# Kernel optimization log

Measured on AMD Instinct MI355X. Metric: run time of the kernel, lower is better.

The kernel has to match this reference:

```python
import jax, jax.numpy as jnp
import numpy as np

S = 100        # sos_token_num
H = 12         # num heads
LY = 3         # number of residual blocks
NEG = -100.0   # attention-bias masking value


def layer_norm(x, w, b, eps=1e-5):
    u = jnp.mean(x, -1, keepdims=True)
    v = jnp.mean((x - u) ** 2, -1, keepdims=True)
    return (x - u) / jnp.sqrt(v + eps) * w + b


def quick_gelu(x):
    return x * jax.nn.sigmoid(1.702 * x)


def l2norm(x, eps=1e-12):
    return x / jnp.maximum(jnp.linalg.norm(x, axis=-1, keepdims=True), eps)


def setup_inputs() -> dict:
    key = jax.random.key(0)
    ks = iter(jax.random.split(key, 32))
    n, c, hh, ww, out_dim = 2, 768, 32, 32, 512
    r = lambda shape, s=1.0: jax.random.normal(next(ks), shape, jnp.float32) * s
    return dict(
        cls_token=r((1, n, c)),
        pix_feat=r((n, c, hh, ww)),
        last_surgery=r((1 + hh * ww, n, c)),
        attn_bias=r((n, 1, S, hh, ww)),
        qkv_w=r((LY, 3 * c, c), 0.02), qkv_b=jnp.zeros((LY, 3 * c)),
        proj_w=r((LY, c, c), 0.02), proj_b=jnp.zeros((LY, c)),
        ln1_w=jnp.ones((LY, c)), ln1_b=jnp.zeros((LY, c)),
        ln2_w=jnp.ones((LY, c)), ln2_b=jnp.zeros((LY, c)),
        fc_w=r((LY, 4 * c, c), 0.02), fc_b=jnp.zeros((LY, 4 * c)),
        fc2_w=r((LY, c, 4 * c), 0.02), fc2_b=jnp.zeros((LY, c)),
        lnp_w=jnp.ones((c,)), lnp_b=jnp.zeros((c,)),
        proj_out=r((c, out_dim), 0.02),
    )


def reference(cls_token, pix_feat, last_surgery, attn_bias,
              qkv_w, qkv_b, proj_w, proj_b,
              ln1_w, ln1_b, ln2_w, ln2_b,
              fc_w, fc_b, fc2_w, fc2_b,
              lnp_w, lnp_b, proj_out):
    n, c, hh, ww = pix_feat.shape
    L = hh * ww
    N = S + 1 + L
    d = c // H
    scale = d ** -0.5

    # ---- assemble token streams (batch-first [n, N, c]) ----
    pix_tok = pix_feat.reshape(n, c, L).transpose(2, 0, 1)          # [L, n, c]
    x = jnp.concatenate([jnp.broadcast_to(cls_token, (S, n, c)), cls_token, pix_tok], 0)
    x_sur = jnp.concatenate([jnp.broadcast_to(last_surgery[0:1], (S, n, c)), last_surgery], 0)
    xo = x.transpose(1, 0, 2)      # 'original' stream  [n, N, c]
    xs = x_sur.transpose(1, 0, 2)  # 'surgery'  stream  [n, N, c]

    # ---- build attention biases (identity downsample: bias already at (h, w)) ----
    base = jnp.zeros((N, N), jnp.float32)
    base = base.at[:, :S].set(NEG)
    base = base.at[jnp.arange(S), jnp.arange(S)].set(0.0)
    base = base.at[:S, S].set(NEG)
    plain = jnp.broadcast_to(base, (n, H, N, N))
    bias = jnp.broadcast_to(attn_bias, (n, H, S, hh, ww)).reshape(n, H, S, L)
    biased = plain.at[:, :, :S, S + 1:].set(bias)   # sos rows attend to pixels via bias

    def attention(t, l):
        # t: [n, N, c] (post-ln_1); returns (surgery_res, ori_res)
        qkv = (t @ qkv_w[l].T + qkv_b[l]).reshape(n, N, 3, H, d).transpose(2, 0, 3, 1, 4)
        q, k, v = qkv[0], qkv[1], qkv[2]   # each [n, H, N, d]
        def attend(q_, k_, mask):
            a = jax.nn.softmax(jnp.einsum('bhnd,bhmd->bhnm', q_, k_) * scale + mask, axis=-1)
            o = jnp.einsum('bhnm,bhmd->bhnd', a, v).transpose(0, 2, 1, 3).reshape(n, N, c)
            return o @ proj_w[l].T + proj_b[l]
        x_ori_res = attend(q, k, biased)   # standard pass, biased mask (attn_mask[0])
        x_res = attend(v, v, plain)        # q = k = v surgery pass (attn_mask[1])
        return x_res, x_ori_res

    for l in range(LY):
        t = layer_norm(xo, ln1_w[l], ln1_b[l])
        res_sur, res_ori = attention(t, l)
        xo = xo + res_ori
        xo = xo + (quick_gelu(layer_norm(xo, ln2_w[l], ln2_b[l]) @ fc_w[l].T + fc_b[l]) @ fc2_w[l].T + fc2_b[l])
        xs = xs + res_sur

    # ---- heads ----
    sos = l2norm(layer_norm(xo[:, :S], lnp_w, lnp_b) @ proj_out)          # [n, S, out]
    img = l2norm(layer_norm(xs[:, S:], lnp_w, lnp_b) @ proj_out)          # [n, 1+L, out]
    img = img[:, 1:, :].transpose(0, 2, 1).reshape(n, proj_out.shape[1], hh, ww)
    return sos, img
```

## Files before the change

kernel.cpp:

```cpp
#include <hip/hip_runtime.h>
#include <math.h>


constexpr int Cc = 768;
constexpr int Ss = 100;
constexpr int Hh = 12;
constexpr int Ll = 1024;
constexpr int Nn = 1125;
constexpr int NB = 2;
constexpr int VTS = 1216;
constexpr float QS = 0.18033688011112042f;
constexpr float LOG2E = 1.4426950408889634f;

typedef unsigned short u16;
typedef unsigned int u32;
typedef __attribute__((ext_vector_type(8))) short short8v;
typedef __attribute__((ext_vector_type(8))) unsigned short ushort8v;
typedef __attribute__((ext_vector_type(4))) float f32x4;
typedef __attribute__((ext_vector_type(4))) unsigned int u32x4;

__device__ inline u16 f2bf(float f) {
  unsigned u = __builtin_bit_cast(unsigned int, f);
  unsigned r = u + 0x7fffu + ((u >> 16) & 1u);
  return (u16)(r >> 16);
}
__device__ inline float bf2f(u16 v) {
  return __builtin_bit_cast(float, (unsigned int)v << 16);
}
__device__ inline unsigned cvtpk(float lo, float hi) {
  unsigned r;
  asm("v_cvt_pk_bf16_f32 %0, %1, %2" : "=v"(r) : "v"(lo), "v"(hi));
  return r;
}
__device__ inline float max3f(float a, float b, float c) {
  float r;
  asm("v_max3_f32 %0, %1, %2, %3" : "=v"(r) : "v"(a), "v"(b), "v"(c));
  return r;
}
__device__ __forceinline__ void gl_lds16(const u16* g, u16* l) {
  __builtin_amdgcn_global_load_lds(
      (const __attribute__((address_space(1))) u32*)g,
      (__attribute__((address_space(3))) u32*)l, 16, 0, 0);
}

__device__ inline int swz(int row, int col) {
  return (row << 6) + ((((col >> 3) ^ (row & 7)) << 3) | (col & 7));
}

__global__ __launch_bounds__(256) void assemble_kernel(
    const float* __restrict__ cls, const float* __restrict__ pix,
    const float* __restrict__ sur, float* __restrict__ xo, float* __restrict__ xs) {
  int idx = blockIdx.x * 256 + (int)threadIdx.x;
  int total = NB * Nn * Cc;
  if (idx >= total) return;
  int ch = idx % Cc;
  int t  = (idx / Cc) % Nn;
  int b  = idx / (Cc * Nn);
  float vo, vs;
  if (t <= Ss) vo = cls[b * Cc + ch];
  else         vo = pix[(size_t)b * Cc * Ll + (size_t)ch * Ll + (t - Ss - 1)];
  if (t < Ss)  vs = sur[b * Cc + ch];
  else         vs = sur[(size_t)(t - Ss) * NB * Cc + b * Cc + ch];
  xo[idx] = vo;
  xs[idx] = vs;
}

constexpr int CN0 = 3 * 2304 * 768;
constexpr int CN1 = 3 * 768 * 768;
constexpr int CN2 = 3 * 3072 * 768;
constexpr int CN3 = 3 * 768 * 3072;
__global__ __launch_bounds__(256) void cvt4_kernel(
    const float* __restrict__ s0, const float* __restrict__ s1,
    const float* __restrict__ s2, const float* __restrict__ s3,
    u16* __restrict__ dst) {
  int i4 = (blockIdx.x * 256 + (int)threadIdx.x) * 4;
  if (i4 >= CN0 + CN1 + CN2 + CN3) return;
  const float* src; int off;
  if (i4 < CN0)             { src = s0; off = i4; }
  else if (i4 < CN0 + CN1)  { src = s1; off = i4 - CN0; }
  else if (i4 < CN0 + CN1 + CN2) { src = s2; off = i4 - CN0 - CN1; }
  else                      { src = s3; off = i4 - CN0 - CN1 - CN2; }
  float4 v = *(const float4*)(src + off);
  *(ushort4*)(dst + i4) = make_ushort4(f2bf(v.x), f2bf(v.y), f2bf(v.z), f2bf(v.w));
}

__global__ __launch_bounds__(256) void transpose_po_kernel(
    const float* __restrict__ in, u16* __restrict__ out) {
  int id = blockIdx.x * 256 + (int)threadIdx.x;
  if (id >= 512 * 768) return;
  int nidx = id / 768, k = id - nidx * 768;
  out[id] = f2bf(in[(size_t)k * 512 + nidx]);
}

__global__ __launch_bounds__(256) void vtrans_kernel(
    const u16* __restrict__ qkv, u16* __restrict__ vtg) {
  __shared__ u16 tile[64][72];
  int tt = blockIdx.x;
  int bh = blockIdx.y;
  int b = bh / Hh, h = bh - b * Hh;
  int tid = (int)threadIdx.x;
  {
    int tl = tid >> 2, c0 = (tid & 3) << 4;
    int tok = tt * 64 + tl;
    int tokc = tok > 1124 ? 1124 : tok;
    const u16* src = qkv + ((size_t)(b * Nn + tokc)) * 2304 + 2 * Cc + h * 64 + c0;
    ushort8v v0 = *(const ushort8v*)src;
    ushort8v v1 = *(const ushort8v*)(src + 8);
    if (tok > 1124) { v0 = (ushort8v)0; v1 = (ushort8v)0; }
    *(ushort8v*)&tile[tl][c0] = v0;
    *(ushort8v*)&tile[tl][c0 + 8] = v1;
  }
  __syncthreads();
  {
    int d = tid >> 2, t0 = (tid & 3) << 4;
    ushort8v o0, o1;
#pragma unroll
    for (int j = 0; j < 8; ++j) { o0[j] = tile[t0 + j][d]; o1[j] = tile[t0 + 8 + j][d]; }
    size_t orow = ((size_t)bh * 64 + d) * VTS + tt * 64 + t0;
    *(ushort8v*)&vtg[orow] = o0;
    *(ushort8v*)&vtg[orow + 8] = o1;
  }
}

__global__ __launch_bounds__(256) void ln_kernel(
    const float* __restrict__ X, const float* __restrict__ w, const float* __restrict__ b,
    u16* __restrict__ Y, int rows_per_b, int row_off) {
  int r = blockIdx.x;
  int bb = r / rows_per_b;
  int i  = r % rows_per_b;
  const float* x = X + ((size_t)bb * Nn + row_off + i) * Cc;
  u16* y = Y + (size_t)r * Cc;
  int tid = (int)threadIdx.x;
  float v0 = x[tid], v1 = x[tid + 256], v2 = x[tid + 512];
  float s = v0 + v1 + v2;
  __shared__ float sbuf[4];
  for (int off = 32; off; off >>= 1) s += __shfl_xor(s, off);
  if ((tid & 63) == 0) sbuf[tid >> 6] = s;
  __syncthreads();
  float mean = (sbuf[0] + sbuf[1] + sbuf[2] + sbuf[3]) * (1.0f / Cc);
  float d0 = v0 - mean, d1 = v1 - mean, d2 = v2 - mean;
  float q = d0 * d0 + d1 * d1 + d2 * d2;
  __syncthreads();
  for (int off = 32; off; off >>= 1) q += __shfl_xor(q, off);
  if ((tid & 63) == 0) sbuf[tid >> 6] = q;
  __syncthreads();
  float var = (sbuf[0] + sbuf[1] + sbuf[2] + sbuf[3]) * (1.0f / Cc);
  float inv = rsqrtf(var + 1e-5f);
  y[tid]       = f2bf(d0 * inv * w[tid]       + b[tid]);
  y[tid + 256] = f2bf(d1 * inv * w[tid + 256] + b[tid + 256]);
  y[tid + 512] = f2bf(d2 * inv * w[tid + 512] + b[tid + 512]);
}

__global__ __launch_bounds__(256) void gemm64_kernel(
    const u16* __restrict__ A0, const u16* __restrict__ A1,
    const u16* __restrict__ B, const float* __restrict__ bias,
    const float* __restrict__ res0, const float* __restrict__ res1,
    float* __restrict__ outf0, float* __restrict__ outf1,
    u16* __restrict__ outb0, u16* __restrict__ outb1,
    int M, int N, int K, int act) {
  __shared__ __align__(16) u16 Als[64 * 64];
  __shared__ __align__(16) u16 Bls[128 * 64];
  int zz = blockIdx.z;
  const u16* A = zz ? A1 : A0;
  const float* res = zz ? res1 : res0;
  float* outf = zz ? outf1 : outf0;
  u16* outb = zz ? outb1 : outb0;
  int tid = (int)threadIdx.x;
  int wave = tid >> 6, lane = tid & 63, g = lane >> 4, li = lane & 15;
  int row0 = blockIdx.y * 64, col0 = blockIdx.x * 128;

  int lr = lane >> 3, lc = (lane & 7) << 3;
  int ar0 = row0 + wave * 16 + lr;      if (ar0 > M - 1) ar0 = M - 1;
  int ar1 = row0 + wave * 16 + 8 + lr;  if (ar1 > M - 1) ar1 = M - 1;
  const u16* as0 = A + (size_t)ar0 * K + lc;
  const u16* as1 = A + (size_t)ar1 * K + lc;
  u16* al0 = &Als[wave * 1024];
  u16* al1 = &Als[wave * 1024 + 512];
  const u16* bs[4]; u16* bl[4];
#pragma unroll
  for (int j = 0; j < 4; ++j) {
    int brow = wave * 32 + j * 8 + lr;
    bs[j] = B + (size_t)(col0 + brow) * K + lc;
    bl[j] = &Bls[(wave * 4 + j) * 512];
  }

  f32x4 acc[4][2];
#pragma unroll
  for (int mi = 0; mi < 4; ++mi)
#pragma unroll
    for (int ni = 0; ni < 2; ++ni) acc[mi][ni] = (f32x4){0.f, 0.f, 0.f, 0.f};

  for (int k0 = 0; k0 < K; k0 += 64) {
    if (k0) __syncthreads();
    gl_lds16(as0 + k0, al0);
    gl_lds16(as1 + k0, al1);
#pragma unroll
    for (int j = 0; j < 4; ++j) gl_lds16(bs[j] + k0, bl[j]);
    __syncthreads();
#pragma unroll
    for (int kc = 0; kc < 2; ++kc) {
      short8v af[4], bfr[2];
#pragma unroll
      for (int mi = 0; mi < 4; ++mi)
        af[mi] = *(const short8v*)&Als[(mi * 16 + li) * 64 + kc * 32 + g * 8];
#pragma unroll
      for (int ni = 0; ni < 2; ++ni)
        bfr[ni] = *(const short8v*)&Bls[(wave * 32 + ni * 16 + li) * 64 + kc * 32 + g * 8];
      __builtin_amdgcn_s_setprio(1);
#pragma unroll
      for (int mi = 0; mi < 4; ++mi)
#pragma unroll
        for (int ni = 0; ni < 2; ++ni)
          acc[mi][ni] = __builtin_amdgcn_mfma_f32_16x16x32_bf16(af[mi], bfr[ni], acc[mi][ni], 0, 0, 0);
      __builtin_amdgcn_s_setprio(0);
    }
  }

#pragma unroll
  for (int mi = 0; mi < 4; ++mi) {
#pragma unroll
    for (int r = 0; r < 4; ++r) {
      int m = row0 + mi * 16 + g * 4 + r;
      if (m >= M) continue;
#pragma unroll
      for (int ni = 0; ni < 2; ++ni) {
        int n = col0 + wave * 32 + ni * 16 + li;
        float v = acc[mi][ni][r];
        if (bias) v += bias[n];
        if (act)  v = v / (1.0f + __expf(-1.702f * v));
        if (res)  v += res[(size_t)m * N + n];
        if (outf) outf[(size_t)m * N + n] = v;
        else      outb[(size_t)m * N + n] = f2bf(v);
      }
    }
  }
}

__global__ __launch_bounds__(256) void attn_kernel(
    const u16* __restrict__ qkv, const u16* __restrict__ vtg,
    const float* __restrict__ abias,
    u16* __restrict__ ao, u16* __restrict__ as_) {
  __shared__ __align__(16) u16 Klds[64 * 64];
  __shared__ __align__(16) u16 Vt[64 * 64];
  int id = (int)blockIdx.x;
  int virt = (id & 7) * 114 + (id >> 3);
  int gid = virt / 19;
  int qt  = virt - gid * 19;
  int z   = gid / 24;
  int bh  = gid - z * 24;
  int b = bh / Hh, h = bh - b * Hh;
  int tid = (int)threadIdx.x;
  int wave = tid >> 6, lane = tid & 63, g = lane >> 4, li = lane & 15;
  bool sosq = qt >= 17;
  u16* outp = z ? as_ : ao;

  int qbase = sosq ? (qt - 17) * 64 + wave * 16 : Ss + qt * 64 + wave * 16;
  int qtok = qbase + li;
  int qcap = sosq ? 99 : 1124;
  if (qtok > qcap) qtok = qcap;
  int qoff = z ? 2 * Cc + h * 64 : h * 64;
  int koff = z ? 2 * Cc + h * 64 : Cc + h * 64;

  short8v qf[2];
  {
    const u16* qp = qkv + ((size_t)b * Nn + qtok) * 2304 + qoff;
#pragma unroll
    for (int kc = 0; kc < 2; ++kc) {
      ushort8v a = *(const ushort8v*)(qp + kc * 32 + g * 8);
      u32x4 w;
#pragma unroll
      for (int jj = 0; jj < 4; ++jj)
        w[jj] = cvtpk(bf2f(a[2 * jj]) * QS, bf2f(a[2 * jj + 1]) * QS);
      qf[kc] = __builtin_bit_cast(short8v, w);
    }
  }

  int skey = tid >> 2;
  int sd0  = (tid & 3) << 4;
  int prow = 16 * (2 * (skey >> 5) + ((skey >> 2) & 1)) + 4 * ((skey >> 3) & 3) + (skey & 3);
  int kK0 = swz(prow, sd0), kK1 = swz(prow, sd0 + 8);
  int vI0 = swz(skey, sd0), vI1 = swz(skey, sd0 + 8);
  const u16* kbase = qkv + (size_t)b * Nn * 2304 + koff + sd0;
  const u16* vbase = vtg + ((size_t)bh * 64 + skey) * VTS + sd0;

  const int KOFF[4] = {0, 4, 32, 36};

  f32x4 oacc[4];
#pragma unroll
  for (int dt = 0; dt < 4; ++dt) oacc[dt] = (f32x4){0.f, 0.f, 0.f, 0.f};
  float mrow = -1e30f, lrow = 0.f;

  int NT = sosq ? 18 : 17;
  for (int kt = 0; kt < NT; ++kt) {
    int t0 = sosq ? (kt == 0 ? (qt - 17) * 64 : 64 * kt + 32) : 96 + 64 * kt;
    __syncthreads();
    {
      int ktok = t0 + skey; if (ktok > 1124) ktok = 1124;
      const u16* kp = kbase + (size_t)ktok * 2304;
      ushort8v k0v = *(const ushort8v*)kp;
      ushort8v k1v = *(const ushort8v*)(kp + 8);
      const u16* vp = vbase + t0;
      ushort8v v0 = *(const ushort8v*)vp;
      ushort8v v1 = *(const ushort8v*)(vp + 8);
      *(ushort8v*)&Klds[kK0] = k0v;
      *(ushort8v*)&Klds[kK1] = k1v;
      *(ushort8v*)&Vt[vI0] = v0;
      *(ushort8v*)&Vt[vI1] = v1;
    }
    __syncthreads();

    f32x4 sacc[4];
#pragma unroll
    for (int nt = 0; nt < 4; ++nt) sacc[nt] = (f32x4){0.f, 0.f, 0.f, 0.f};
    __builtin_amdgcn_s_setprio(1);
#pragma unroll
    for (int kc = 0; kc < 2; ++kc) {
#pragma unroll
      for (int nt = 0; nt < 4; ++nt) {
        short8v kb = *(const short8v*)&Klds[swz(nt * 16 + li, kc * 32 + g * 8)];
        sacc[nt] = __builtin_amdgcn_mfma_f32_16x16x32_bf16(kb, qf[kc], sacc[nt], 0, 0, 0);
      }
    }
    __builtin_amdgcn_s_setprio(0);

    int tg = t0 + 8 * g;
    if (!sosq) {
      if (kt == 0) {
#pragma unroll
        for (int nt = 0; nt < 4; ++nt)
#pragma unroll
          for (int r = 0; r < 4; ++r)
            if (tg + KOFF[nt] + r < 100) sacc[nt][r] = -1e30f;
      } else if (kt == 16) {
#pragma unroll
        for (int nt = 0; nt < 4; ++nt)
#pragma unroll
          for (int r = 0; r < 4; ++r)
            if (tg + KOFF[nt] + r > 1124) sacc[nt][r] = -1e30f;
      }
    } else {
      if (kt == 0) {
#pragma unroll
        for (int nt = 0; nt < 4; ++nt)
#pragma unroll
          for (int r = 0; r < 4; ++r)
            if (tg + KOFF[nt] + r != qtok) sacc[nt][r] = -1e30f;
      } else if (z == 0) {
        const float* bp = abias + ((size_t)b * Ss + qtok) * Ll;
#pragma unroll
        for (int nt = 0; nt < 4; ++nt)
#pragma unroll
          for (int r = 0; r < 4; ++r) {
            int tok = tg + KOFF[nt] + r;
            int bi = tok - 101; bi = bi < 0 ? 0 : bi; bi = bi > 1023 ? 1023 : bi;
            float bv = bp[bi];
            bool bad = (tok < 101) | (tok > 1124);
            sacc[nt][r] = bad ? -1e30f : fmaf(bv, LOG2E, sacc[nt][r]);
          }
      } else {
#pragma unroll
        for (int nt = 0; nt < 4; ++nt)
#pragma unroll
          for (int r = 0; r < 4; ++r) {
            int tok = tg + KOFF[nt] + r;
            if ((tok < 101) | (tok > 1124)) sacc[nt][r] = -1e30f;
          }
      }
    }

    float rmax = max3f(sacc[0][0], sacc[0][1], sacc[0][2]);
    rmax = max3f(rmax, sacc[0][3], sacc[1][0]);
    rmax = max3f(rmax, sacc[1][1], sacc[1][2]);
    rmax = max3f(rmax, sacc[1][3], sacc[2][0]);
    rmax = max3f(rmax, sacc[2][1], sacc[2][2]);
    rmax = max3f(rmax, sacc[2][3], sacc[3][0]);
    rmax = max3f(rmax, sacc[3][1], sacc[3][2]);
    rmax = fmaxf(rmax, sacc[3][3]);
    rmax = fmaxf(rmax, __shfl_xor(rmax, 16));
    rmax = fmaxf(rmax, __shfl_xor(rmax, 32));
    float mnew = fmaxf(mrow, rmax);
    float fac = __builtin_amdgcn_exp2f(mrow - mnew);
    mrow = mnew;
    float psum = 0.f;
#pragma unroll
    for (int nt = 0; nt < 4; ++nt)
#pragma unroll
      for (int r = 0; r < 4; ++r) {
        float e = __builtin_amdgcn_exp2f(sacc[nt][r] - mnew);
        sacc[nt][r] = e;
        psum += e;
      }
    psum += __shfl_xor(psum, 16);
    psum += __shfl_xor(psum, 32);
    lrow = lrow * fac + psum;
#pragma unroll
    for (int dt = 0; dt < 4; ++dt) oacc[dt] *= fac;

    __builtin_amdgcn_s_setprio(1);
#pragma unroll
    for (int kcp = 0; kcp < 2; ++kcp) {
      u32x4 pwv;
#pragma unroll
      for (int w = 0; w < 4; ++w) {
        int nt = 2 * kcp + (w >> 1);
        int r0 = (w & 1) * 2;
        pwv[w] = cvtpk(sacc[nt][r0], sacc[nt][r0 + 1]);
      }
      short8v pb = __builtin_bit_cast(short8v, pwv);
#pragma unroll
      for (int dt = 0; dt < 4; ++dt) {
        short8v va = *(const short8v*)&Vt[swz(dt * 16 + li, kcp * 32 + g * 8)];
        oacc[dt] = __builtin_amdgcn_mfma_f32_16x16x32_bf16(va, pb, oacc[dt], 0, 0, 0);
      }
    }
    __builtin_amdgcn_s_setprio(0);
  }

  int tok = qbase + li;
  if (tok <= qcap) {
    float inv = 1.0f / lrow;
    u16* op = outp + ((size_t)b * Nn + tok) * Cc + h * 64 + g * 4;
#pragma unroll
    for (int dt = 0; dt < 4; ++dt) {
      unsigned lo = cvtpk(oacc[dt][0] * inv, oacc[dt][1] * inv);
      unsigned hi = cvtpk(oacc[dt][2] * inv, oacc[dt][3] * inv);
      uint2 o2; o2.x = lo; o2.y = hi;
      *(uint2*)(op + dt * 16) = o2;
    }
  }
}

__global__ __launch_bounds__(256) void l2norm_sos_kernel(
    const float* __restrict__ Xp, float* __restrict__ out) {
  int r = blockIdx.x;
  int tid = (int)threadIdx.x;
  const float* x = Xp + (size_t)r * 512;
  float v0 = x[tid], v1 = x[tid + 256];
  float s = v0 * v0 + v1 * v1;
  __shared__ float sbuf[4];
  for (int off = 32; off; off >>= 1) s += __shfl_xor(s, off);
  if ((tid & 63) == 0) sbuf[tid >> 6] = s;
  __syncthreads();
  float tot = sbuf[0] + sbuf[1] + sbuf[2] + sbuf[3];
  float inv = 1.0f / fmaxf(sqrtf(tot), 1e-12f);
  out[(size_t)r * 512 + tid]       = v0 * inv;
  out[(size_t)r * 512 + tid + 256] = v1 * inv;
}

__global__ __launch_bounds__(256) void l2norm_img_kernel(
    const float* __restrict__ Xp, float* __restrict__ out) {
  int r = blockIdx.x;
  int b = r / 1025, ti = r % 1025;
  int tid = (int)threadIdx.x;
  const float* x = Xp + (size_t)r * 512;
  float v0 = x[tid], v1 = x[tid + 256];
  float s = v0 * v0 + v1 * v1;
  __shared__ float sbuf[4];
  for (int off = 32; off; off >>= 1) s += __shfl_xor(s, off);
  if ((tid & 63) == 0) sbuf[tid >> 6] = s;
  __syncthreads();
  float tot = sbuf[0] + sbuf[1] + sbuf[2] + sbuf[3];
  if (ti == 0) return;
  float inv = 1.0f / fmaxf(sqrtf(tot), 1e-12f);
  float* o = out + (size_t)b * 512 * 1024 + (ti - 1);
  o[(size_t)tid * 1024]         = v0 * inv;
  o[(size_t)(tid + 256) * 1024] = v1 * inv;
}

extern "C" void kernel_launch(void* const* d_in, const int* in_sizes, int n_in,
                              void* d_out, int out_size, void* d_ws, size_t ws_size,
                              hipStream_t stream) {
  const float* cls      = (const float*)d_in[0];
  const float* pix      = (const float*)d_in[1];
  const float* sur      = (const float*)d_in[2];
  const float* abias    = (const float*)d_in[3];
  const float* qkv_w    = (const float*)d_in[4];
  const float* qkv_b    = (const float*)d_in[5];
  const float* proj_w   = (const float*)d_in[6];
  const float* proj_b   = (const float*)d_in[7];
  const float* ln1_w    = (const float*)d_in[8];
  const float* ln1_b    = (const float*)d_in[9];
  const float* ln2_w    = (const float*)d_in[10];
  const float* ln2_b    = (const float*)d_in[11];
  const float* fc_w     = (const float*)d_in[12];
  const float* fc_b     = (const float*)d_in[13];
  const float* fc2_w    = (const float*)d_in[14];
  const float* fc2_b    = (const float*)d_in[15];
  const float* lnp_w    = (const float*)d_in[16];
  const float* lnp_b    = (const float*)d_in[17];
  const float* proj_o   = (const float*)d_in[18];
  float* out = (float*)d_out;

  const size_t SZ = (size_t)NB * Nn * Cc;
  float* xo      = (float*)d_ws;
  float* xs      = xo + SZ;
  float* head_pj = xs + SZ;
  u16* tln_bf = (u16*)(head_pj + 2250 * 512);
  u16* act_bf = tln_bf + (size_t)2250 * 768;
  u16* ao_bf  = act_bf + (size_t)2250 * 3072;
  u16* as_bf  = ao_bf + (size_t)2250 * 768;
  u16* wq_bf  = as_bf + (size_t)2250 * 768;
  u16* wp_bf  = wq_bf + (size_t)CN0;
  u16* wf_bf  = wp_bf + (size_t)CN1;
  u16* w2_bf  = wf_bf + (size_t)CN2;
  u16* wo_bf  = w2_bf + (size_t)CN3;
  u16* vtg    = wo_bf + (size_t)512 * 768;

  assemble_kernel<<<6750, 256, 0, stream>>>(cls, pix, sur, xo, xs);
  cvt4_kernel<<<20736, 256, 0, stream>>>(qkv_w, proj_w, fc_w, fc2_w, wq_bf);
  transpose_po_kernel<<<1536, 256, 0, stream>>>(proj_o, wo_bf);

  for (int l = 0; l < 3; ++l) {
    ln_kernel<<<2250, 256, 0, stream>>>(xo, ln1_w + l * 768, ln1_b + l * 768, tln_bf, Nn, 0);
    gemm64_kernel<<<dim3(18, 36, 1), 256, 0, stream>>>(
        tln_bf, tln_bf, wq_bf + (size_t)l * 2304 * 768, qkv_b + l * 2304,
        nullptr, nullptr, nullptr, nullptr, act_bf, act_bf, 2250, 2304, 768, 0);
    vtrans_kernel<<<dim3(19, 24), 256, 0, stream>>>(act_bf, vtg);
    attn_kernel<<<912, 256, 0, stream>>>(act_bf, vtg, abias, ao_bf, as_bf);
    gemm64_kernel<<<dim3(6, 36, 2), 256, 0, stream>>>(
        ao_bf, as_bf, wp_bf + (size_t)l * 768 * 768, proj_b + l * 768,
        xo, xs, xo, xs, nullptr, nullptr, 2250, 768, 768, 0);
    ln_kernel<<<2250, 256, 0, stream>>>(xo, ln2_w + l * 768, ln2_b + l * 768, tln_bf, Nn, 0);
    gemm64_kernel<<<dim3(24, 36, 1), 256, 0, stream>>>(
        tln_bf, tln_bf, wf_bf + (size_t)l * 3072 * 768, fc_b + l * 3072,
        nullptr, nullptr, nullptr, nullptr, act_bf, act_bf, 2250, 3072, 768, 1);
    gemm64_kernel<<<dim3(6, 36, 1), 256, 0, stream>>>(
        act_bf, act_bf, w2_bf + (size_t)l * 768 * 3072, fc2_b + l * 768,
        xo, xo, xo, xo, nullptr, nullptr, 2250, 768, 3072, 0);
  }

  ln_kernel<<<200, 256, 0, stream>>>(xo, lnp_w, lnp_b, tln_bf, 100, 0);
  ln_kernel<<<2050, 256, 0, stream>>>(xs, lnp_w, lnp_b, tln_bf + 200 * 768, 1025, 100);
  gemm64_kernel<<<dim3(4, 36, 1), 256, 0, stream>>>(
      tln_bf, tln_bf, wo_bf, nullptr,
      nullptr, nullptr, head_pj, head_pj, nullptr, nullptr, 2250, 512, 768, 0);
  l2norm_sos_kernel<<<200, 256, 0, stream>>>(head_pj, out);
  l2norm_img_kernel<<<2050, 256, 0, stream>>>(head_pj + 200 * 512, out + 102400);
}
```

Measured before the change: 800.9 us.

## Double-buffer LDS tiles in GEMM and attention kernels to overlap loads

```diff
diff --git a/kernel.cpp b/kernel.cpp
--- a/kernel.cpp
+++ b/kernel.cpp
@@ -158,8 +158,8 @@
     float* __restrict__ outf0, float* __restrict__ outf1,
     u16* __restrict__ outb0, u16* __restrict__ outb1,
     int M, int N, int K, int act) {
-  __shared__ __align__(16) u16 Als[64 * 64];
-  __shared__ __align__(16) u16 Bls[128 * 64];
+  __shared__ __align__(16) u16 Als[2][64 * 64];
+  __shared__ __align__(16) u16 Bls[2][128 * 64];
   int zz = blockIdx.z;
   const u16* A = zz ? A1 : A0;
   const float* res = zz ? res1 : res0;
@@ -174,14 +174,13 @@
   int ar1 = row0 + wave * 16 + 8 + lr;  if (ar1 > M - 1) ar1 = M - 1;
   const u16* as0 = A + (size_t)ar0 * K + lc;
   const u16* as1 = A + (size_t)ar1 * K + lc;
-  u16* al0 = &Als[wave * 1024];
-  u16* al1 = &Als[wave * 1024 + 512];
-  const u16* bs[4]; u16* bl[4];
+  int aoff0 = wave * 1024, aoff1 = wave * 1024 + 512;
+  const u16* bs[4]; int boff[4];
 #pragma unroll
   for (int j = 0; j < 4; ++j) {
     int brow = wave * 32 + j * 8 + lr;
     bs[j] = B + (size_t)(col0 + brow) * K + lc;
-    bl[j] = &Bls[(wave * 4 + j) * 512];
+    boff[j] = (wave * 4 + j) * 512;
   }
 
   f32x4 acc[4][2];
@@ -190,22 +189,31 @@
 #pragma unroll
     for (int ni = 0; ni < 2; ++ni) acc[mi][ni] = (f32x4){0.f, 0.f, 0.f, 0.f};
 
-  for (int k0 = 0; k0 < K; k0 += 64) {
-    if (k0) __syncthreads();
-    gl_lds16(as0 + k0, al0);
-    gl_lds16(as1 + k0, al1);
-#pragma unroll
-    for (int j = 0; j < 4; ++j) gl_lds16(bs[j] + k0, bl[j]);
+  gl_lds16(as0, &Als[0][aoff0]);
+  gl_lds16(as1, &Als[0][aoff1]);
+#pragma unroll
+  for (int j = 0; j < 4; ++j) gl_lds16(bs[j], &Bls[0][boff[j]]);
+
+  int nt = K >> 6;
+  for (int t = 0; t < nt; ++t) {
+    int cur = t & 1;
     __syncthreads();
+    if (t + 1 < nt) {
+      int k0n = (t + 1) << 6;
+      gl_lds16(as0 + k0n, &Als[cur ^ 1][aoff0]);
+      gl_lds16(as1 + k0n, &Als[cur ^ 1][aoff1]);
+#pragma unroll
+      for (int j = 0; j < 4; ++j) gl_lds16(bs[j] + k0n, &Bls[cur ^ 1][boff[j]]);
+    }
 #pragma unroll
     for (int kc = 0; kc < 2; ++kc) {
       short8v af[4], bfr[2];
 #pragma unroll
       for (int mi = 0; mi < 4; ++mi)
-        af[mi] = *(const short8v*)&Als[(mi * 16 + li) * 64 + kc * 32 + g * 8];
+        af[mi] = *(const short8v*)&Als[cur][(mi * 16 + li) * 64 + kc * 32 + g * 8];
 #pragma unroll
       for (int ni = 0; ni < 2; ++ni)
-        bfr[ni] = *(const short8v*)&Bls[(wave * 32 + ni * 16 + li) * 64 + kc * 32 + g * 8];
+        bfr[ni] = *(const short8v*)&Bls[cur][(wave * 32 + ni * 16 + li) * 64 + kc * 32 + g * 8];
       __builtin_amdgcn_s_setprio(1);
 #pragma unroll
       for (int mi = 0; mi < 4; ++mi)
@@ -240,8 +248,8 @@
     const u16* __restrict__ qkv, const u16* __restrict__ vtg,
     const float* __restrict__ abias,
     u16* __restrict__ ao, u16* __restrict__ as_) {
-  __shared__ __align__(16) u16 Klds[64 * 64];
-  __shared__ __align__(16) u16 Vt[64 * 64];
+  __shared__ __align__(16) u16 Klds[2][64 * 64];
+  __shared__ __align__(16) u16 Vt[2][64 * 64];
   int id = (int)blockIdx.x;
   int virt = (id & 7) * 114 + (id >> 3);
   int gid = virt / 19;
@@ -291,23 +299,33 @@
   float mrow = -1e30f, lrow = 0.f;
 
   int NT = sosq ? 18 : 17;
+  int qdiag = (qt - 17) * 64;
+
+  ushort8v kr0, kr1, vr0, vr1;
+#define TBASE(kt) (sosq ? ((kt) == 0 ? qdiag : 64 * (kt) + 32) : 96 + 64 * (kt))
+#define STAGE(kt)                                                  \
+  {                                                                \
+    int t0n = TBASE(kt);                                           \
+    int ktok = t0n + skey; if (ktok > 1124) ktok = 1124;           \
+    const u16* kp = kbase + (size_t)ktok * 2304;                   \
+    kr0 = *(const ushort8v*)kp;                                    \
+    kr1 = *(const ushort8v*)(kp + 8);                              \
+    const u16* vp = vbase + t0n;                                   \
+    vr0 = *(const ushort8v*)vp;                                    \
+    vr1 = *(const ushort8v*)(vp + 8);                              \
+  }
+
+  STAGE(0);
+  *(ushort8v*)&Klds[0][kK0] = kr0;
+  *(ushort8v*)&Klds[0][kK1] = kr1;
+  *(ushort8v*)&Vt[0][vI0]   = vr0;
+  *(ushort8v*)&Vt[0][vI1]   = vr1;
+
   for (int kt = 0; kt < NT; ++kt) {
-    int t0 = sosq ? (kt == 0 ? (qt - 17) * 64 : 64 * kt + 32) : 96 + 64 * kt;
+    int cur = kt & 1;
+    int t0 = TBASE(kt);
     __syncthreads();
-    {
-      int ktok = t0 + skey; if (ktok > 1124) ktok = 1124;
-      const u16* kp = kbase + (size_t)ktok * 2304;
-      ushort8v k0v = *(const ushort8v*)kp;
-      ushort8v k1v = *(const ushort8v*)(kp + 8);
-      const u16* vp = vbase + t0;
-      ushort8v v0 = *(const ushort8v*)vp;
-      ushort8v v1 = *(const ushort8v*)(vp + 8);
-      *(ushort8v*)&Klds[kK0] = k0v;
-      *(ushort8v*)&Klds[kK1] = k1v;
-      *(ushort8v*)&Vt[vI0] = v0;
-      *(ushort8v*)&Vt[vI1] = v1;
-    }
-    __syncthreads();
+    if (kt + 1 < NT) STAGE(kt + 1);
 
     f32x4 sacc[4];
 #pragma unroll
@@ -317,7 +335,7 @@
     for (int kc = 0; kc < 2; ++kc) {
 #pragma unroll
       for (int nt = 0; nt < 4; ++nt) {
-        short8v kb = *(const short8v*)&Klds[swz(nt * 16 + li, kc * 32 + g * 8)];
+        short8v kb = *(const short8v*)&Klds[cur][swz(nt * 16 + li, kc * 32 + g * 8)];
         sacc[nt] = __builtin_amdgcn_mfma_f32_16x16x32_bf16(kb, qf[kc], sacc[nt], 0, 0, 0);
       }
     }
@@ -409,12 +427,21 @@
       short8v pb = __builtin_bit_cast(short8v, pwv);
 #pragma unroll
       for (int dt = 0; dt < 4; ++dt) {
-        short8v va = *(const short8v*)&Vt[swz(dt * 16 + li, kcp * 32 + g * 8)];
+        short8v va = *(const short8v*)&Vt[cur][swz(dt * 16 + li, kcp * 32 + g * 8)];
         oacc[dt] = __builtin_amdgcn_mfma_f32_16x16x32_bf16(va, pb, oacc[dt], 0, 0, 0);
       }
     }
     __builtin_amdgcn_s_setprio(0);
-  }
+
+    if (kt + 1 < NT) {
+      *(ushort8v*)&Klds[cur ^ 1][kK0] = kr0;
+      *(ushort8v*)&Klds[cur ^ 1][kK1] = kr1;
+      *(ushort8v*)&Vt[cur ^ 1][vI0]   = vr0;
+      *(ushort8v*)&Vt[cur ^ 1][vI1]   = vr1;
+    }
+  }
+#undef STAGE
+#undef TBASE
 
   int tok = qbase + li;
   if (tok <= qcap) {
```

Result: slower. 821.5 us (+2.6%).
